# Optimization experiments

Measured on AMD Instinct MI355X. Metric: run time of the kernel, lower is better.

## Reference

```python
import jax, jax.numpy as jnp
import numpy as np

N = 8192   # samples
D = 128    # number of variables / towers (dims[0])
D1 = 128   # hidden width (dims[1])


def setup_inputs() -> dict:
    key = jax.random.key(0)
    k_x, k_w0, k_w1, k_b1 = jax.random.split(key, 4)
    x = jax.random.normal(k_x, (N, D), dtype=jnp.float32)
    # Layer 0: one Linear(D -> D1) per tower -> batched weight [D_towers, D1, D_in]
    W0 = jax.random.normal(k_w0, (D, D1, D), dtype=jnp.float32) * (1.0 / np.sqrt(D))
    # NOTEARS init: zero self-edge column i of tower i, zero layer-0 biases
    idx = jnp.arange(D)
    W0 = W0.at[idx, :, idx].set(0.0)
    b0 = jnp.zeros((D, D1), dtype=jnp.float32)
    # Layer 1: Linear(D1 -> 1) per tower
    W1 = jax.random.normal(k_w1, (D, 1, D1), dtype=jnp.float32) * (1.0 / np.sqrt(D1))
    b1 = jax.random.normal(k_b1, (D, 1), dtype=jnp.float32) * 0.05
    return {"x": x, "W0": W0, "b0": b0, "W1": W1, "b1": b1}


def reference(x, W0, b0, W1, b1):
    # binary-input check from the original forward
    binary = jnp.all((x == 0) | (x == 1))
    # Layer 0 for all D towers at once: [n,d] x [k,h,d] -> [n,k,h]
    h = jax.nn.sigmoid(jnp.einsum('nd,khd->nkh', x, W0) + b0)
    # Layer 1 (output dim 1 per tower): [n,k,h] x [k,h] -> [n,k]
    out = jnp.einsum('nkh,kh->nk', h, W1[:, 0, :]) + b1[:, 0]
    out = jnp.where(binary, jax.nn.sigmoid(out), out)
    return out
```

## Files before the change

### kernel.cpp

```cpp
#include <hip/hip_runtime.h>
#include <hip/hip_bf16.h>
#include <stdint.h>

#define N_SAMP 8192
#define D_TOW  128
#define D_HID  128
#define LOG2E  1.442695040888963f

typedef __bf16 bf16x8 __attribute__((ext_vector_type(8)));
typedef float  f32x4  __attribute__((ext_vector_type(4)));

__device__ __forceinline__ ushort f2bf(float f) {
  union { float f; uint32_t u; } c; c.f = f;
  uint32_t u = c.u;
  return (ushort)((u + 0x7FFFu + ((u >> 16) & 1u)) >> 16);
}

__global__ __launch_bounds__(256) void prep_kernel(
    const float* __restrict__ x, const float* __restrict__ w0,
    ushort* __restrict__ xb, ushort* __restrict__ w0b, int* __restrict__ flag) {
  const int NX4 = (N_SAMP * D_TOW) / 4;
  const int NW4 = (D_TOW * D_HID * D_TOW) / 4;
  int t = blockIdx.x * blockDim.x + threadIdx.x;
  if (t < NX4) {
    float4 v = ((const float4*)x)[t];
    bool bad = !(((v.x == 0.f) || (v.x == 1.f)) &&
                 ((v.y == 0.f) || (v.y == 1.f)) &&
                 ((v.z == 0.f) || (v.z == 1.f)) &&
                 ((v.w == 0.f) || (v.w == 1.f)));
    ushort4 o;
    o.x = f2bf(v.x); o.y = f2bf(v.y); o.z = f2bf(v.z); o.w = f2bf(v.w);
    ((ushort4*)xb)[t] = o;
    if (__ballot(bad) != 0ull && (threadIdx.x & 63) == 0) *flag = 1;
  } else if (t < NX4 + NW4) {
    int j = t - NX4;
    float4 v = ((const float4*)w0)[j];
    ushort4 o;
    o.x = f2bf(v.x); o.y = f2bf(v.y); o.z = f2bf(v.z); o.w = f2bf(v.w);
    ((ushort4*)w0b)[j] = o;
  }
}

__device__ __forceinline__ void g2l16(const void* g, void* l) {
  __builtin_amdgcn_global_load_lds(
      (const __attribute__((address_space(1))) void*)g,
      (__attribute__((address_space(3))) void*)l, 16, 0, 0);
}

__global__ __launch_bounds__(256, 3) void towers_kernel(
    const ushort* __restrict__ xb, const ushort* __restrict__ w0b,
    const float* __restrict__ b0, const float* __restrict__ w1,
    const float* __restrict__ b1, const int* __restrict__ flag,
    float* __restrict__ out) {
  __shared__ __align__(16) ushort sX[64 * 128];
  __shared__ float sG[4][64][17];

  int bid = blockIdx.x;
  int xcd = bid & 7;
  int r = bid >> 3;
  int kg4 = r & 3;
  int chunk = r >> 2;
  int k0 = xcd * 16 + kg4 * 4;
  int n0 = chunk * 64;

  int tid = threadIdx.x;
  int lane = tid & 63;
  int wave = tid >> 6;
  int q = lane >> 4;
  int cl = lane & 15;

  const ushort* xg = xb + n0 * 128;
  const ushort* wg = w0b + k0 * (128 * 128);

  int aOff[2];
#pragma unroll
  for (int f = 0; f < 2; ++f)
    aOff[f] = (wave * 32 + f * 16 + cl) * 128 + q * 8;

  bf16x8 aA[4][2], aB[4][2];
#pragma unroll
  for (int t = 0; t < 4; ++t)
#pragma unroll
    for (int f = 0; f < 2; ++f)
      aA[t][f] = *(const bf16x8*)(wg + aOff[f] + t * 32);

#pragma unroll
  for (int i = 0; i < 4; ++i) {
    int base = wave * 4096 + i * 1024;
    int row = wave * 16 + i * 4 + q;
    int c = cl ^ (row & 15);
    g2l16(xg + row * 128 + c * 8, (char*)sX + base);
  }
  __syncthreads();

  int flagv = *flag;

  bf16x8 b[4][4];
#pragma unroll
  for (int t = 0; t < 4; ++t)
#pragma unroll
    for (int nf = 0; nf < 4; ++nf)
      b[t][nf] = *(const bf16x8*)(
          (const char*)sX + (nf * 16 + cl) * 256 + (((t * 4 + q) ^ cl) << 4));

#define TOWER_BODY(J, ACUR, ANEXT, DO_PRE)                                     \
  {                                                                            \
    f32x4 acc[2][4];                                                           \
    _Pragma("unroll") for (int hf = 0; hf < 2; ++hf)                           \
        _Pragma("unroll") for (int nf = 0; nf < 4; ++nf)                       \
            acc[hf][nf] = (f32x4){0.f, 0.f, 0.f, 0.f};                         \
    _Pragma("unroll") for (int t = 0; t < 4; ++t)                              \
        _Pragma("unroll") for (int hf = 0; hf < 2; ++hf)                       \
            _Pragma("unroll") for (int nf = 0; nf < 4; ++nf)                   \
                acc[hf][nf] = __builtin_amdgcn_mfma_f32_16x16x32_bf16(         \
                    ACUR[t][hf], b[t][nf], acc[hf][nf], 0, 0, 0);              \
    if (DO_PRE) {                                                              \
      const ushort* wgn = wg + (J + 1) * (128 * 128);                          \
      _Pragma("unroll") for (int t = 0; t < 4; ++t)                            \
          _Pragma("unroll") for (int f = 0; f < 2; ++f)                        \
              ANEXT[t][f] = *(const bf16x8*)(wgn + aOff[f] + t * 32);          \
    }                                                                          \
    float s[4] = {0.f, 0.f, 0.f, 0.f};                                         \
    _Pragma("unroll") for (int hf = 0; hf < 2; ++hf) {                         \
      int h = (k0 + J) * 128 + wave * 32 + hf * 16 + q * 4;                    \
      f32x4 bb = *(const f32x4*)&b0[h];                                        \
      f32x4 wv = *(const f32x4*)&w1[h];                                        \
      f32x4 bbc;                                                               \
      _Pragma("unroll") for (int rr = 0; rr < 4; ++rr)                         \
          bbc[rr] = bb[rr] * -LOG2E;                                           \
      _Pragma("unroll") for (int nf = 0; nf < 4; ++nf)                         \
          _Pragma("unroll") for (int rr = 0; rr < 4; ++rr) {                   \
        float e = __builtin_amdgcn_exp2f(                                      \
            __builtin_fmaf(acc[hf][nf][rr], -LOG2E, bbc[rr]));                 \
        s[nf] = __builtin_fmaf(wv[rr], __builtin_amdgcn_rcpf(1.0f + e), s[nf]);\
      }                                                                        \
    }                                                                          \
    _Pragma("unroll") for (int nf = 0; nf < 4; ++nf)                           \
        sG[J][nf * 16 + cl][wave * 4 + q] = s[nf];                             \
  }

  TOWER_BODY(0, aA, aB, 1)
  TOWER_BODY(1, aB, aA, 1)
  TOWER_BODY(2, aA, aB, 1)
  TOWER_BODY(3, aB, aA, 0)
#undef TOWER_BODY

  __syncthreads();

  {
    int n = tid & 63;
    int j = tid >> 6;
    float v = b1[k0 + j];
#pragma unroll
    for (int p = 0; p < 16; ++p)
      v += sG[j][n][p];
    if (flagv != 1) {
      float e = __builtin_amdgcn_exp2f(v * -LOG2E);
      v = __builtin_amdgcn_rcpf(1.0f + e);
    }
    out[(size_t)(n0 + n) * D_TOW + k0 + j] = v;
  }
}

extern "C" void kernel_launch(void* const* d_in, const int* in_sizes, int n_in,
                              void* d_out, int out_size, void* d_ws, size_t ws_size,
                              hipStream_t stream) {
  const float* x  = (const float*)d_in[0];
  const float* w0 = (const float*)d_in[1];
  const float* b0 = (const float*)d_in[2];
  const float* w1 = (const float*)d_in[3];
  const float* b1 = (const float*)d_in[4];
  float* out = (float*)d_out;

  char* ws = (char*)d_ws;
  int* flag = (int*)ws;
  ushort* xb  = (ushort*)(ws + 1024);
  ushort* w0b = (ushort*)(ws + 1024 + N_SAMP * D_TOW * 2);

  int total4 = (N_SAMP * D_TOW + D_TOW * D_HID * D_TOW) / 4;
  prep_kernel<<<total4 / 256, 256, 0, stream>>>(x, w0, xb, w0b, flag);

  towers_kernel<<<4096, 256, 0, stream>>>(xb, w0b, b0, w1, b1, flag, out);
}
```

Baseline: 145.2 us.

## Software-pipeline tower MFMA bursts with epilogues using two accumulator sets

Restructures the per-tower loop so two accumulator sets alternate: the MFMA burst for the next tower is issued before the sigmoid/reduce epilogue of the previous one, overlapping transcendental ALU work with matrix work. The X fragments are now re-read from LDS for each burst instead of staying in registers for the whole kernel. Occupancy is lowered from 3 to 2 blocks per SIMD budget to make room for the extra accumulators. The bias add is also restructured slightly. The trade-off is more LDS reads and lower occupancy in exchange for better intra-wave overlap.

```diff
diff --git a/kernel.cpp b/kernel.cpp
--- a/kernel.cpp
+++ b/kernel.cpp
@@ -47,7 +47,7 @@
       (__attribute__((address_space(3))) void*)l, 16, 0, 0);
 }
 
-__global__ __launch_bounds__(256, 3) void towers_kernel(
+__global__ __launch_bounds__(256, 2) void towers_kernel(
     const ushort* __restrict__ xb, const ushort* __restrict__ w0b,
     const float* __restrict__ b0, const float* __restrict__ w1,
     const float* __restrict__ b1, const int* __restrict__ flag,
@@ -78,11 +78,53 @@
     aOff[f] = (wave * 32 + f * 16 + cl) * 128 + q * 8;
 
   bf16x8 aA[4][2], aB[4][2];
-#pragma unroll
-  for (int t = 0; t < 4; ++t)
-#pragma unroll
-    for (int f = 0; f < 2; ++f)
-      aA[t][f] = *(const bf16x8*)(wg + aOff[f] + t * 32);
+  f32x4 acc0[2][4], acc1[2][4];
+
+#define PREF(J, AFR)                                                           \
+  do {                                                                         \
+    const ushort* wp = wg + (J) * (128 * 128);                                 \
+    _Pragma("unroll") for (int t = 0; t < 4; ++t)                              \
+        _Pragma("unroll") for (int f = 0; f < 2; ++f)                          \
+            AFR[t][f] = *(const bf16x8*)(wp + aOff[f] + t * 32);               \
+  } while (0)
+
+#define BURST(ACC, AFR)                                                        \
+  do {                                                                         \
+    _Pragma("unroll") for (int hf = 0; hf < 2; ++hf)                           \
+        _Pragma("unroll") for (int nf = 0; nf < 4; ++nf)                       \
+            ACC[hf][nf] = (f32x4){0.f, 0.f, 0.f, 0.f};                         \
+    _Pragma("unroll") for (int t = 0; t < 4; ++t) {                            \
+      bf16x8 bfr[4];                                                           \
+      int ch = ((t * 4 + q) ^ cl) << 4;                                        \
+      _Pragma("unroll") for (int nf = 0; nf < 4; ++nf)                         \
+          bfr[nf] = *(const bf16x8*)(                                          \
+              (const char*)sX + (nf * 16 + cl) * 256 + ch);                    \
+      _Pragma("unroll") for (int hf = 0; hf < 2; ++hf)                         \
+          _Pragma("unroll") for (int nf = 0; nf < 4; ++nf)                     \
+              ACC[hf][nf] = __builtin_amdgcn_mfma_f32_16x16x32_bf16(           \
+                  AFR[t][hf], bfr[nf], ACC[hf][nf], 0, 0, 0);                  \
+    }                                                                          \
+  } while (0)
+
+#define EPI(J, ACC)                                                            \
+  do {                                                                         \
+    float s[4] = {0.f, 0.f, 0.f, 0.f};                                         \
+    _Pragma("unroll") for (int hf = 0; hf < 2; ++hf) {                         \
+      int h = (k0 + (J)) * 128 + wave * 32 + hf * 16 + q * 4;                  \
+      f32x4 bb = *(const f32x4*)&b0[h];                                        \
+      f32x4 wv = *(const f32x4*)&w1[h];                                        \
+      _Pragma("unroll") for (int nf = 0; nf < 4; ++nf)                         \
+          _Pragma("unroll") for (int rr = 0; rr < 4; ++rr) {                   \
+        float e = __builtin_amdgcn_exp2f(__builtin_fmaf(                       \
+            ACC[hf][nf][rr] + bb[rr], -LOG2E, 0.f));                           \
+        s[nf] = __builtin_fmaf(wv[rr], __builtin_amdgcn_rcpf(1.0f + e), s[nf]);\
+      }                                                                        \
+    }                                                                          \
+    _Pragma("unroll") for (int nf = 0; nf < 4; ++nf)                           \
+        sG[J][nf * 16 + cl][wave * 4 + q] = s[nf];                             \
+  } while (0)
+
+  PREF(0, aA);
 
 #pragma unroll
   for (int i = 0; i < 4; ++i) {
@@ -95,55 +137,21 @@
 
   int flagv = *flag;
 
-  bf16x8 b[4][4];
-#pragma unroll
-  for (int t = 0; t < 4; ++t)
-#pragma unroll
-    for (int nf = 0; nf < 4; ++nf)
-      b[t][nf] = *(const bf16x8*)(
-          (const char*)sX + (nf * 16 + cl) * 256 + (((t * 4 + q) ^ cl) << 4));
+  PREF(1, aB);
+  BURST(acc0, aA);
+  BURST(acc1, aB);
+  PREF(2, aA);
+  EPI(0, acc0);
+  BURST(acc0, aA);
+  PREF(3, aB);
+  EPI(1, acc1);
+  BURST(acc1, aB);
+  EPI(2, acc0);
+  EPI(3, acc1);
 
-#define TOWER_BODY(J, ACUR, ANEXT, DO_PRE)                                     \
-  {                                                                            \
-    f32x4 acc[2][4];                                                           \
-    _Pragma("unroll") for (int hf = 0; hf < 2; ++hf)                           \
-        _Pragma("unroll") for (int nf = 0; nf < 4; ++nf)                       \
-            acc[hf][nf] = (f32x4){0.f, 0.f, 0.f, 0.f};                         \
-    _Pragma("unroll") for (int t = 0; t < 4; ++t)                              \
-        _Pragma("unroll") for (int hf = 0; hf < 2; ++hf)                       \
-            _Pragma("unroll") for (int nf = 0; nf < 4; ++nf)                   \
-                acc[hf][nf] = __builtin_amdgcn_mfma_f32_16x16x32_bf16(         \
-                    ACUR[t][hf], b[t][nf], acc[hf][nf], 0, 0, 0);              \
-    if (DO_PRE) {                                                              \
-      const ushort* wgn = wg + (J + 1) * (128 * 128);                          \
-      _Pragma("unroll") for (int t = 0; t < 4; ++t)                            \
-          _Pragma("unroll") for (int f = 0; f < 2; ++f)                        \
-              ANEXT[t][f] = *(const bf16x8*)(wgn + aOff[f] + t * 32);          \
-    }                                                                          \
-    float s[4] = {0.f, 0.f, 0.f, 0.f};                                         \
-    _Pragma("unroll") for (int hf = 0; hf < 2; ++hf) {                         \
-      int h = (k0 + J) * 128 + wave * 32 + hf * 16 + q * 4;                    \
-      f32x4 bb = *(const f32x4*)&b0[h];                                        \
-      f32x4 wv = *(const f32x4*)&w1[h];                                        \
-      f32x4 bbc;                                                               \
-      _Pragma("unroll") for (int rr = 0; rr < 4; ++rr)                         \
-          bbc[rr] = bb[rr] * -LOG2E;                                           \
-      _Pragma("unroll") for (int nf = 0; nf < 4; ++nf)                         \
-          _Pragma("unroll") for (int rr = 0; rr < 4; ++rr) {                   \
-        float e = __builtin_amdgcn_exp2f(                                      \
-            __builtin_fmaf(acc[hf][nf][rr], -LOG2E, bbc[rr]));                 \
-        s[nf] = __builtin_fmaf(wv[rr], __builtin_amdgcn_rcpf(1.0f + e), s[nf]);\
-      }                                                                        \
-    }                                                                          \
-    _Pragma("unroll") for (int nf = 0; nf < 4; ++nf)                           \
-        sG[J][nf * 16 + cl][wave * 4 + q] = s[nf];                             \
-  }
-
-  TOWER_BODY(0, aA, aB, 1)
-  TOWER_BODY(1, aB, aA, 1)
-  TOWER_BODY(2, aA, aB, 1)
-  TOWER_BODY(3, aB, aA, 0)
-#undef TOWER_BODY
+#undef PREF
+#undef BURST
+#undef EPI
 
   __syncthreads();
 
```

After: 145.1 us. No clear change (-0.0%).
